# Kernel optimization log

Hardware: AMD Instinct MI355X
Metric: run time of the kernel (lower is better)

Reference implementation:

```python
import jax, jax.numpy as jnp
import numpy as np

B, N, K = 4, 4096, 10   # batch, num points, ED_nsample
SA, ED = 128, 4          # SA_conv_out, ED_conv_out


def _bn_pack(key, C):
    # rows: gamma, beta, running_mean, running_var (eval-mode BatchNorm1d)
    kg, kb, km, kv = jax.random.split(key, 4)
    g = 1.0 + 0.1 * jax.random.normal(kg, (C,))
    b = 0.1 * jax.random.normal(kb, (C,))
    m = 0.1 * jax.random.normal(km, (C,))
    v = jax.random.uniform(kv, (C,), minval=0.5, maxval=1.5)
    return jnp.stack([g, b, m, v])


def _conv_params(key, o, c):
    kw, kb = jax.random.split(key)
    return (jax.random.normal(kw, (o, c)) * (1.0 / np.sqrt(c)),
            0.01 * jax.random.normal(kb, (o,)))


def setup_inputs() -> dict:
    key = jax.random.key(0)
    ks = iter(jax.random.split(key, 32))
    inp = {}
    inp['pointcloud'] = jax.random.normal(next(ks), (B, N, 3), dtype=jnp.float32)
    inp['h1'] = jax.random.normal(next(ks), (B, SA, N), dtype=jnp.float32)      # Pointnet_Backbone output
    inp['h2'] = jax.random.normal(next(ks), (B, 1024, N), dtype=jnp.float32)    # DGCNN output
    shapes = {'dg1': (256, 1024), 'dg2': (64, 256), 'dg3': (32, 64),
              'c1': (512, 160), 'c2': (256, 512), 'c3': (128, 256), 'f': (128, 132)}
    for name, (o, c) in shapes.items():
        W, b = _conv_params(next(ks), o, c)
        inp['W_' + name], inp['b_' + name] = W, b
        inp['bn_' + name] = _bn_pack(next(ks), o)
    inp['W_ed1'] = jax.random.normal(next(ks), (ED, 3)) * 0.5
    inp['b_ed1'] = 0.01 * jax.random.normal(next(ks), (ED,))
    inp['W_ed2'] = jax.random.normal(next(ks), (ED, ED)) * 0.5
    inp['b_ed2'] = 0.01 * jax.random.normal(next(ks), (ED,))
    inp['numpoints'] = N
    return inp


def _bn1d(x, p, eps=1e-5):
    # x: [B, C, N]; p rows: gamma, beta, mean, var
    g, b, m, v = p
    inv = g * jax.lax.rsqrt(v + eps)
    return x * inv[:, None] + (b - m * inv)[:, None]


def _conv1(x, W, b):
    # 1x1 Conv1d == channel matmul. x: [B,C,N], W: [O,C]
    return jnp.einsum('oc,bcn->bon', W, x) + b[:, None]


def reference(pointcloud, h1, h2,
              W_dg1, b_dg1, bn_dg1, W_dg2, b_dg2, bn_dg2, W_dg3, b_dg3, bn_dg3,
              W_c1, b_c1, bn_c1, W_c2, b_c2, bn_c2, W_c3, b_c3, bn_c3,
              W_f, b_f, bn_f, W_ed1, b_ed1, W_ed2, b_ed2, numpoints):
    relu = jax.nn.relu
    xyz = pointcloud[..., :3]  # [B,N,3]

    # DGCNN feature reduction: 1024 -> 256 -> 64 -> 32
    h2_ = relu(_bn1d(_conv1(h2, W_dg1, b_dg1), bn_dg1))
    h2_ = relu(_bn1d(_conv1(h2_, W_dg2, b_dg2), bn_dg2))
    h2_ = relu(_bn1d(_conv1(h2_, W_dg3, b_dg3), bn_dg3))

    # fused feature: 160 -> 512 -> 256 -> 128
    f = jnp.concatenate([h1, h2_], axis=1)
    f_ = relu(_bn1d(_conv1(f, W_c1, b_c1), bn_c1))
    f_ = relu(_bn1d(_conv1(f_, W_c2, b_c2), bn_c2))
    f_ = relu(_bn1d(_conv1(f_, W_c3, b_c3), bn_c3))

    # knn_point: K nearest neighbors of each point within its cloud
    sq = jnp.sum(xyz * xyz, axis=-1)  # [B,N]
    d = sq[:, :, None] + sq[:, None, :] - 2.0 * jnp.einsum('bnd,bmd->bnm', xyz, xyz)
    _, idx = jax.lax.top_k(-d, K)  # [B,N,K]
    nbr = jax.vmap(lambda p, i: p[i])(xyz, idx)  # [B,N,K,3]

    # per-point 3x3 covariance + eigenvalues
    c = nbr - jnp.mean(nbr, axis=2, keepdims=True)
    cov = jnp.einsum('bnki,bnkj->bnij', c, c) / K  # [B,N,3,3]
    ev = jnp.linalg.eigvalsh(cov)  # [B,N,3] ascending

    # sub3_ED: Linear(3,4) -> ReLU -> Linear(4,4)
    ef = relu(ev @ W_ed1.T + b_ed1) @ W_ed2.T + b_ed2  # [B,N,4]
    ef_t = ef.transpose(0, 2, 1)  # [B,4,N]

    z = jnp.concatenate([f_, ef_t], axis=1)  # [B,132,N]
    z_ = relu(_bn1d(_conv1(z, W_f, b_f), bn_f))  # [B,128,N]
    return (xyz, z_, h1, h2_, ef_t)
```

## Files before the change

kernel.cpp:

```cpp
#include <hip/hip_runtime.h>
#include <hip/hip_bf16.h>
#include <math.h>

typedef __hip_bfloat16 bf16;

#define BB 4
#define NN 4096
#define KNB 10
#define KQ 8
#define KS 32
#define KC (NN / KS)
#define KCAP 64

typedef __bf16 bfv8 __attribute__((ext_vector_type(8)));
typedef float  f32x4 __attribute__((ext_vector_type(4)));

__device__ __forceinline__ float ldT(const float* p) { return *p; }
__device__ __forceinline__ float ldT(const bf16* p)  { return __bfloat162float(*p); }
__device__ __forceinline__ void  stT(float* p, float v) { *p = v; }
__device__ __forceinline__ void  stT(bf16* p,  float v) { *p = __float2bfloat16(v); }

__device__ __forceinline__ unsigned short f2us(float x) {
  union { bf16 h; unsigned short u; } cv;
  cv.h = __float2bfloat16(x);
  return cv.u;
}

__device__ __forceinline__ void ld8bits(const float* p, unsigned short* s) {
  const float4 a = *(const float4*)p;
  const float4 b = *(const float4*)(p + 4);
  s[0] = f2us(a.x); s[1] = f2us(a.y); s[2] = f2us(a.z); s[3] = f2us(a.w);
  s[4] = f2us(b.x); s[5] = f2us(b.y); s[6] = f2us(b.z); s[7] = f2us(b.w);
}
__device__ __forceinline__ void ld8bits(const bf16* p, unsigned short* s) {
  const uint2 a = *(const uint2*)p;
  const uint2 b = *(const uint2*)(p + 4);
  s[0] = a.x & 0xffff; s[1] = a.x >> 16; s[2] = a.y & 0xffff; s[3] = a.y >> 16;
  s[4] = b.x & 0xffff; s[5] = b.x >> 16; s[6] = b.y & 0xffff; s[7] = b.y >> 16;
}

__device__ __forceinline__ bfv8 ldfrag(const unsigned short* p) {
  union { uint4 u; bfv8 v; } t;
  t.u = *(const uint4*)p;
  return t.v;
}

__global__ void k_sniff(const unsigned int* __restrict__ pcw, int* __restrict__ flag) {
  if (blockIdx.x == 0 && threadIdx.x == 0) {
    int hits = 0;
    for (int i = 0; i < 64; ++i) {
      unsigned int e = (pcw[i] >> 7) & 0xFF;
      if (e >= 100 && e <= 140) ++hits;
    }
    *flag = (hits >= 40) ? 1 : 0;
  }
}

template <class TI, class TO>
__global__ void k_prep(const int* __restrict__ flag, int want,
                       const TI* __restrict__ pc, float* __restrict__ xyz,
                       float4* __restrict__ pts4, TO* __restrict__ out0) {
  if (flag && *flag != want) return;
  int i = blockIdx.x * blockDim.x + threadIdx.x;
  if (i >= BB * NN) return;
  float x = ldT(pc + i * 3 + 0), y = ldT(pc + i * 3 + 1), z = ldT(pc + i * 3 + 2);
  xyz[i * 3 + 0] = x; xyz[i * 3 + 1] = y; xyz[i * 3 + 2] = z;
  const float nrm = fmaf(x, x, fmaf(y, y, z * z));
  pts4[i] = make_float4(x, y, z, nrm);
  stT(out0 + i * 3 + 0, x); stT(out0 + i * 3 + 1, y); stT(out0 + i * 3 + 2, z);
}

template <class TI, class TO>
__global__ void k_h1(const int* __restrict__ flag, int want,
                     const TI* __restrict__ h1, TO* __restrict__ out2,
                     bf16* __restrict__ fbuf) {
  if (flag && *flag != want) return;
  int i = blockIdx.x * blockDim.x + threadIdx.x;
  const int per = 128 * NN;
  if (i >= BB * per) return;
  float v = ldT(h1 + i);
  stT(out2 + i, v);
  int b = i / per, r = i - b * per;
  fbuf[(size_t)b * 160 * NN + r] = __float2bfloat16(v);
}

__global__ __launch_bounds__(256, 8) void k_knn(const float4* __restrict__ pts4,
                                                int* __restrict__ idxout) {
  __shared__ float sminb[KS][KQ];
  __shared__ float stau[KQ];
  __shared__ float sd[KQ][KCAP];
  __shared__ int   si[KQ][KCAP];
  __shared__ unsigned int scnt[KQ];
  const int tid = threadIdx.x;
  const int q = tid & (KQ - 1);
  const int s = tid >> 3;
  const int n = blockIdx.x * KQ + q;
  const int b = blockIdx.y;
  const float4* pb = pts4 + (size_t)b * NN;
  const float4 pq = pb[n];
  const float xn = pq.x, yn = pq.y, zn = pq.z, sn = pq.w;
  if (tid < KQ) scnt[tid] = 0u;

  const float4* cp = pb + s * KC;
  float mv[8];
  #pragma unroll
  for (int u = 0; u < 8; ++u) mv[u] = 1e30f;
  for (int j = 0; j < KC; j += 8) {
    #pragma unroll
    for (int u = 0; u < 8; ++u) {
      const float4 c = cp[j + u];
      const float dot = fmaf(xn, c.x, fmaf(yn, c.y, zn * c.z));
      const float d = (sn + c.w) - 2.0f * dot;
      mv[u] = fminf(mv[u], d);
    }
  }
  {
    const float a0 = fminf(fminf(mv[0], mv[1]), fminf(mv[2], mv[3]));
    const float a1 = fminf(fminf(mv[4], mv[5]), fminf(mv[6], mv[7]));
    sminb[s][q] = fminf(a0, a1);
  }
  __syncthreads();

  if (tid < KQ) {
    float arr[KNB];
    #pragma unroll
    for (int t = 0; t < KNB; ++t) arr[t] = 1e30f;
    #pragma unroll
    for (int ss = 0; ss < KS; ++ss) {
      const float v = sminb[ss][tid];
      if (v < arr[KNB - 1]) {
        arr[KNB - 1] = v;
        #pragma unroll
        for (int t = KNB - 1; t > 0; --t)
          if (arr[t] < arr[t - 1]) { const float tm = arr[t]; arr[t] = arr[t - 1]; arr[t - 1] = tm; }
      }
    }
    stau[tid] = arr[KNB - 1];
  }
  __syncthreads();
  const float tau = stau[q];

  for (int j = 0; j < KC; j += 4) {
    #pragma unroll
    for (int u = 0; u < 4; ++u) {
      const float4 c = cp[j + u];
      const float dot = fmaf(xn, c.x, fmaf(yn, c.y, zn * c.z));
      const float d = (sn + c.w) - 2.0f * dot;
      if (d <= tau) {
        const unsigned int pos = atomicAdd(&scnt[q], 1u);
        if (pos < KCAP) { sd[q][pos] = d; si[q][pos] = s * KC + j + u; }
      }
    }
  }
  __syncthreads();

  if (tid < KQ) {
    const int qq = tid;
    const int nq = blockIdx.x * KQ + qq;
    int* op = idxout + ((size_t)b * NN + nq) * KNB;
    const unsigned int m = scnt[qq];
    float dk[KNB]; int ik[KNB];
    #pragma unroll
    for (int t = 0; t < KNB; ++t) { dk[t] = 1e30f; ik[t] = NN; }
    if (m <= KCAP) {
      for (unsigned int e = 0; e < m; ++e) {
        const float d = sd[qq][e];
        const int j = si[qq][e];
        if (d < dk[KNB - 1] || (d == dk[KNB - 1] && j < ik[KNB - 1])) {
          dk[KNB - 1] = d; ik[KNB - 1] = j;
          #pragma unroll
          for (int t = KNB - 1; t > 0; --t) {
            if (dk[t] < dk[t - 1] || (dk[t] == dk[t - 1] && ik[t] < ik[t - 1])) {
              const float td = dk[t]; dk[t] = dk[t - 1]; dk[t - 1] = td;
              const int ti = ik[t]; ik[t] = ik[t - 1]; ik[t - 1] = ti;
            }
          }
        }
      }
    } else {
      const float4 pQ = pb[nq];
      for (int j = 0; j < NN; ++j) {
        const float4 c = pb[j];
        const float dot = fmaf(pQ.x, c.x, fmaf(pQ.y, c.y, pQ.z * c.z));
        const float d = (pQ.w + c.w) - 2.0f * dot;
        if (d < dk[KNB - 1] || (d == dk[KNB - 1] && j < ik[KNB - 1])) {
          dk[KNB - 1] = d; ik[KNB - 1] = j;
          #pragma unroll
          for (int t = KNB - 1; t > 0; --t) {
            if (dk[t] < dk[t - 1] || (dk[t] == dk[t - 1] && ik[t] < ik[t - 1])) {
              const float td = dk[t]; dk[t] = dk[t - 1]; dk[t - 1] = td;
              const int ti = ik[t]; ik[t] = ik[t - 1]; ik[t - 1] = ti;
            }
          }
        }
      }
    }
    #pragma unroll
    for (int t = 0; t < KNB; ++t) op[t] = ik[t];
  }
}

template <class TP, class TO>
__global__ void k_ef(const int* __restrict__ flag, int want,
                     const float* __restrict__ xyz, const int* __restrict__ idxin,
                     const TP* __restrict__ W1, const TP* __restrict__ b1,
                     const TP* __restrict__ W2, const TP* __restrict__ b2,
                     TO* __restrict__ out4, bf16* __restrict__ zbuf) {
  if (flag && *flag != want) return;
  int i = blockIdx.x * blockDim.x + threadIdx.x;
  if (i >= BB * NN) return;
  int b = i / NN, n = i - b * NN;
  const float* xb = xyz + (size_t)b * NN * 3;
  const int* id = idxin + (size_t)i * KNB;
  double px[KNB], py[KNB], pz[KNB];
  double mx = 0, my = 0, mz = 0;
  #pragma unroll
  for (int k = 0; k < KNB; ++k) {
    int j = id[k];
    px[k] = (double)xb[j * 3 + 0];
    py[k] = (double)xb[j * 3 + 1];
    pz[k] = (double)xb[j * 3 + 2];
    mx += px[k]; my += py[k]; mz += pz[k];
  }
  mx /= KNB; my /= KNB; mz /= KNB;
  double c00 = 0, c01 = 0, c02 = 0, c11 = 0, c12 = 0, c22 = 0;
  #pragma unroll
  for (int k = 0; k < KNB; ++k) {
    double dx = px[k] - mx, dy = py[k] - my, dz = pz[k] - mz;
    c00 += dx * dx; c01 += dx * dy; c02 += dx * dz;
    c11 += dy * dy; c12 += dy * dz; c22 += dz * dz;
  }
  c00 /= KNB; c01 /= KNB; c02 /= KNB; c11 /= KNB; c12 /= KNB; c22 /= KNB;
  double e0, e1, e2;
  {
    double p1 = c01 * c01 + c02 * c02 + c12 * c12;
    double q = (c00 + c11 + c22) / 3.0;
    double d0 = c00 - q, d1 = c11 - q, d2 = c22 - q;
    double p2 = d0 * d0 + d1 * d1 + d2 * d2 + 2.0 * p1;
    if (p2 <= 0.0) {
      e0 = e1 = e2 = q;
    } else {
      double p = sqrt(p2 / 6.0);
      double ip = 1.0 / p;
      double b00 = d0 * ip, b11 = d1 * ip, b22 = d2 * ip;
      double b01 = c01 * ip, b02 = c02 * ip, b12 = c12 * ip;
      double det = b00 * (b11 * b22 - b12 * b12)
                 - b01 * (b01 * b22 - b12 * b02)
                 + b02 * (b01 * b12 - b11 * b02);
      double r = 0.5 * det;
      r = fmin(1.0, fmax(-1.0, r));
      double phi = acos(r) / 3.0;
      double lmax = q + 2.0 * p * cos(phi);
      double lmin = q + 2.0 * p * cos(phi + 2.0943951023931953);
      e0 = lmin; e2 = lmax; e1 = 3.0 * q - lmax - lmin;
    }
  }
  float ev0 = (float)e0, ev1 = (float)e1, ev2 = (float)e2;
  float h[4];
  #pragma unroll
  for (int o = 0; o < 4; ++o) {
    float t = ev0 * ldT(W1 + o * 3 + 0) + ev1 * ldT(W1 + o * 3 + 1)
            + ev2 * ldT(W1 + o * 3 + 2) + ldT(b1 + o);
    h[o] = fmaxf(t, 0.f);
  }
  #pragma unroll
  for (int j = 0; j < 4; ++j) {
    float t = h[0] * ldT(W2 + j * 4 + 0) + h[1] * ldT(W2 + j * 4 + 1)
            + h[2] * ldT(W2 + j * 4 + 2) + h[3] * ldT(W2 + j * 4 + 3)
            + ldT(b2 + j);
    stT(out4 + ((size_t)b * 4 + j) * NN + n, t);
    zbuf[((size_t)b * 132 + 128 + j) * NN + n] = __float2bfloat16(t);
  }
}

template <class TX, class TP, class TO>
__global__ __launch_bounds__(256) void k_gemm(
    const int* __restrict__ flag, int want,
    const TX* __restrict__ X, int C,
    const TP* __restrict__ W, const TP* __restrict__ bias,
    const TP* __restrict__ bn, int O,
    TO* __restrict__ Yout, int YRo, int yoffo,
    bf16* __restrict__ Ybuf, int YRb, int yoffb) {
  if (flag && *flag != want) return;
  __shared__ __align__(16) unsigned short Ws[64][72];
  __shared__ __align__(16) unsigned short Xs[64][72];
  const int tid  = threadIdx.x;
  const int lane = tid & 63;
  const int wv   = tid >> 6;
  const int wr = wv >> 1, wc = wv & 1;
  const int l15 = lane & 15, lg = lane >> 4;
  const int nBase = blockIdx.x * 64;
  const int oBase = blockIdx.y * 64;
  const int b = blockIdx.z;
  const TX* Xb = X + (size_t)b * C * NN;

  f32x4 acc[2][2];
  #pragma unroll
  for (int m = 0; m < 2; ++m)
    #pragma unroll
    for (int n = 0; n < 2; ++n) acc[m][n] = (f32x4){0.f, 0.f, 0.f, 0.f};

  const int wo  = tid >> 3;
  const int wc0 = (tid & 7) << 3;
  const int xc  = tid >> 3;
  const int xn0 = (tid & 7) << 3;

  for (int cb = 0; cb < C; cb += 64) {
    #pragma unroll
    for (int h = 0; h < 2; ++h) {
      const int o  = wo + h * 32;
      const int go = oBase + o, gc = cb + wc0;
      const int crem = C - gc;
      unsigned short s[8];
      if (go < O && crem >= 8) {
        ld8bits(W + (size_t)go * C + gc, s);
      } else {
        #pragma unroll
        for (int j = 0; j < 8; ++j)
          s[j] = (go < O && j < crem) ? f2us(ldT(W + (size_t)go * C + gc + j))
                                      : (unsigned short)0;
      }
      uint4 u;
      u.x = (unsigned)s[0] | ((unsigned)s[1] << 16);
      u.y = (unsigned)s[2] | ((unsigned)s[3] << 16);
      u.z = (unsigned)s[4] | ((unsigned)s[5] << 16);
      u.w = (unsigned)s[6] | ((unsigned)s[7] << 16);
      *(uint4*)&Ws[o][wc0] = u;
    }
    #pragma unroll
    for (int h = 0; h < 2; ++h) {
      const int c  = xc + h * 32;
      const int gc = cb + c;
      unsigned short s[8];
      if (gc < C) {
        ld8bits(Xb + (size_t)gc * NN + nBase + xn0, s);
      } else {
        #pragma unroll
        for (int j = 0; j < 8; ++j) s[j] = 0;
      }
      const int xcol = c ^ xn0;
      #pragma unroll
      for (int j = 0; j < 8; ++j) Xs[xn0 + j][xcol] = s[j];
    }
    __syncthreads();
    #pragma unroll
    for (int kk = 0; kk < 2; ++kk) {
      bfv8 af[2], xf[2];
      #pragma unroll
      for (int m = 0; m < 2; ++m)
        af[m] = ldfrag(&Ws[wr * 32 + m * 16 + l15][kk * 32 + lg * 8]);
      #pragma unroll
      for (int n = 0; n < 2; ++n) {
        const int nl  = wc * 32 + n * 16 + l15;
        const int col = (kk * 32 + lg * 8) ^ (((nl >> 3) & 7) << 3);
        xf[n] = ldfrag(&Xs[nl][col]);
      }
      #pragma unroll
      for (int m = 0; m < 2; ++m)
        #pragma unroll
        for (int n = 0; n < 2; ++n)
          acc[m][n] = __builtin_amdgcn_mfma_f32_16x16x32_bf16(af[m], xf[n], acc[m][n], 0, 0, 0);
    }
    __syncthreads();
  }

  #pragma unroll
  for (int m = 0; m < 2; ++m) {
    const int ob = oBase + wr * 32 + m * 16 + lg * 4;
    #pragma unroll
    for (int r = 0; r < 4; ++r) {
      const int oo = ob + r;
      if (oo >= O) continue;
      const float bc  = ldT(bias + oo);
      const float g   = ldT(bn + oo);
      const float bbv = ldT(bn + O + oo);
      const float mm  = ldT(bn + 2 * O + oo);
      const float vv  = ldT(bn + 3 * O + oo);
      const float inv = g / sqrtf(vv + 1e-5f);
      const float sh  = bbv - mm * inv;
      #pragma unroll
      for (int n = 0; n < 2; ++n) {
        const int nn2 = nBase + wc * 32 + n * 16 + l15;
        const float rv = fmaxf((acc[m][n][r] + bc) * inv + sh, 0.f);
        if (Yout) stT(Yout + ((size_t)b * YRo + yoffo + oo) * NN + nn2, rv);
        if (Ybuf) Ybuf[((size_t)b * YRb + yoffb + oo) * NN + nn2] = __float2bfloat16(rv);
      }
    }
  }
}

template <class TI>
static void launch_prep(int want, const int* flag, void* const* d_in, void* d_out,
                        hipStream_t stream, float* xyz, float4* pts4) {
  typedef TI TO;
  const TI* pc = (const TI*)d_in[0];
  TO* out0 = (TO*)d_out;
  k_prep<TI, TO><<<dim3((BB * NN + 255) / 256), 256, 0, stream>>>(flag, want, pc, xyz, pts4, out0);
}

template <class TI>
static void launch_rest(int want, const int* flag,
                        void* const* d_in, void* d_out, hipStream_t stream,
                        float* xyz, int* idx,
                        bf16* t512, bf16* t256, bf16* t64, bf16* fbuf, bf16* zbuf) {
  typedef TI TO;
  const TI* h1    = (const TI*)d_in[1];
  const TI* h2    = (const TI*)d_in[2];
  const TI* W_dg1 = (const TI*)d_in[3];  const TI* b_dg1 = (const TI*)d_in[4];  const TI* bn_dg1 = (const TI*)d_in[5];
  const TI* W_dg2 = (const TI*)d_in[6];  const TI* b_dg2 = (const TI*)d_in[7];  const TI* bn_dg2 = (const TI*)d_in[8];
  const TI* W_dg3 = (const TI*)d_in[9];  const TI* b_dg3 = (const TI*)d_in[10]; const TI* bn_dg3 = (const TI*)d_in[11];
  const TI* W_c1  = (const TI*)d_in[12]; const TI* b_c1  = (const TI*)d_in[13]; const TI* bn_c1  = (const TI*)d_in[14];
  const TI* W_c2  = (const TI*)d_in[15]; const TI* b_c2  = (const TI*)d_in[16]; const TI* bn_c2  = (const TI*)d_in[17];
  const TI* W_c3  = (const TI*)d_in[18]; const TI* b_c3  = (const TI*)d_in[19]; const TI* bn_c3  = (const TI*)d_in[20];
  const TI* W_f   = (const TI*)d_in[21]; const TI* b_f   = (const TI*)d_in[22]; const TI* bn_f   = (const TI*)d_in[23];
  const TI* W_ed1 = (const TI*)d_in[24]; const TI* b_ed1 = (const TI*)d_in[25];
  const TI* W_ed2 = (const TI*)d_in[26]; const TI* b_ed2 = (const TI*)d_in[27];

  TO* out  = (TO*)d_out;
  TO* out1 = out + 49152;
  TO* out2 = out1 + 2097152;
  TO* out3 = out2 + 2097152;
  TO* out4 = out3 + 524288;

  dim3 blk(256);
  k_h1<TI, TO><<<dim3((BB * 128 * NN + 255) / 256), 256, 0, stream>>>(flag, want, h1, out2, fbuf);
  k_gemm<TI, TI, TO><<<dim3(64, 4, BB), blk, 0, stream>>>(flag, want, h2, 1024, W_dg1, b_dg1, bn_dg1, 256,
                                                          (TO*)nullptr, 0, 0, t256, 256, 0);
  k_gemm<bf16, TI, TO><<<dim3(64, 1, BB), blk, 0, stream>>>(flag, want, t256, 256, W_dg2, b_dg2, bn_dg2, 64,
                                                            (TO*)nullptr, 0, 0, t64, 64, 0);
  k_gemm<bf16, TI, TO><<<dim3(64, 1, BB), blk, 0, stream>>>(flag, want, t64, 64, W_dg3, b_dg3, bn_dg3, 32,
                                                            out3, 32, 0, fbuf, 160, 128);
  k_gemm<bf16, TI, TO><<<dim3(64, 8, BB), blk, 0, stream>>>(flag, want, fbuf, 160, W_c1, b_c1, bn_c1, 512,
                                                            (TO*)nullptr, 0, 0, t512, 512, 0);
  k_ef<TI, TO><<<dim3((BB * NN + 255) / 256), 256, 0, stream>>>(flag, want, xyz, idx, W_ed1, b_ed1, W_ed2, b_ed2, out4, zbuf);
  k_gemm<bf16, TI, TO><<<dim3(64, 4, BB), blk, 0, stream>>>(flag, want, t512, 512, W_c2, b_c2, bn_c2, 256,
                                                            (TO*)nullptr, 0, 0, t256, 256, 0);
  k_gemm<bf16, TI, TO><<<dim3(64, 2, BB), blk, 0, stream>>>(flag, want, t256, 256, W_c3, b_c3, bn_c3, 128,
                                                            (TO*)nullptr, 0, 0, zbuf, 132, 0);
  k_gemm<bf16, TI, TO><<<dim3(64, 2, BB), blk, 0, stream>>>(flag, want, zbuf, 132, W_f, b_f, bn_f, 128,
                                                            out1, 128, 0, (bf16*)nullptr, 0, 0);
}

extern "C" void kernel_launch(void* const* d_in, const int* in_sizes, int n_in,
                              void* d_out, int out_size, void* d_ws, size_t ws_size,
                              hipStream_t stream) {
  char* ws = (char*)d_ws;
  int*    flag = (int*)(ws + 0);
  float*  xyz  = (float*)(ws + 1024);
  int*    idx  = (int*)(ws + 328704);
  bf16*   t512 = (bf16*)(ws + 1048576);
  bf16*   t256 = (bf16*)(ws + 17825792);
  bf16*   t64  = (bf16*)(ws + 26214400);
  bf16*   fbuf = (bf16*)(ws + 28311552);
  bf16*   zbuf = (bf16*)(ws + 33554432);
  float4* pts4 = (float4*)(ws + 1048576);

  int mode = -1;
  if (in_sizes) {
    if (in_sizes[0] == (int)(BB * NN * 3 * sizeof(float))) mode = 0;
    else if (in_sizes[0] == (int)(BB * NN * 3 * sizeof(bf16))) mode = 1;
  }

  if (mode < 0) {
    k_sniff<<<1, 64, 0, stream>>>((const unsigned int*)d_in[0], flag);
    launch_prep<float>(0, flag, d_in, d_out, stream, xyz, pts4);
    launch_prep<bf16>(1, flag, d_in, d_out, stream, xyz, pts4);
  } else if (mode == 0) {
    launch_prep<float>(0, nullptr, d_in, d_out, stream, xyz, pts4);
  } else {
    launch_prep<bf16>(1, nullptr, d_in, d_out, stream, xyz, pts4);
  }

  k_knn<<<dim3(NN / KQ, BB), 256, 0, stream>>>(pts4, idx);

  if (mode != 1) launch_rest<float>(0, mode < 0 ? flag : nullptr, d_in, d_out, stream,
                                    xyz, idx, t512, t256, t64, fbuf, zbuf);
  if (mode != 0) launch_rest<bf16>(1, mode < 0 ? flag : nullptr, d_in, d_out, stream,
                                   xyz, idx, t512, t256, t64, fbuf, zbuf);
}
```

Measured before the change: 394.1 us.

## Restructure kNN so each thread scans strided candidates against all block queries

The kNN kernel now has each thread load a strided candidate point once and compute distances against all 8 queries of the block held in registers. Before, each thread handled one query over a contiguous chunk. Candidate loads become coalesced and each load is reused across queries, cutting global or cache traffic. In exchange, the threshold pass now reduces 256 per-thread minima per query instead of 32, serialized in 8 threads. Register pressure also rises, so launch bounds drop from 8 to 6 blocks per CU.

```diff
diff --git a/kernel.cpp b/kernel.cpp
--- a/kernel.cpp
+++ b/kernel.cpp
@@ -8,8 +8,6 @@
 #define NN 4096
 #define KNB 10
 #define KQ 8
-#define KS 32
-#define KC (NN / KS)
 #define KCAP 64
 
 typedef __bf16 bfv8 __attribute__((ext_vector_type(8)));
@@ -84,71 +82,76 @@
   fbuf[(size_t)b * 160 * NN + r] = __float2bfloat16(v);
 }
 
-__global__ __launch_bounds__(256, 8) void k_knn(const float4* __restrict__ pts4,
+__global__ __launch_bounds__(256, 6) void k_knn(const float4* __restrict__ pts4,
                                                 int* __restrict__ idxout) {
-  __shared__ float sminb[KS][KQ];
+  __shared__ float smin[256][KQ + 1];
   __shared__ float stau[KQ];
   __shared__ float sd[KQ][KCAP];
   __shared__ int   si[KQ][KCAP];
   __shared__ unsigned int scnt[KQ];
+  __shared__ float4 sq[KQ];
   const int tid = threadIdx.x;
-  const int q = tid & (KQ - 1);
-  const int s = tid >> 3;
-  const int n = blockIdx.x * KQ + q;
   const int b = blockIdx.y;
+  const int nBase = blockIdx.x * KQ;
   const float4* pb = pts4 + (size_t)b * NN;
-  const float4 pq = pb[n];
-  const float xn = pq.x, yn = pq.y, zn = pq.z, sn = pq.w;
-  if (tid < KQ) scnt[tid] = 0u;
-
-  const float4* cp = pb + s * KC;
-  float mv[8];
-  #pragma unroll
-  for (int u = 0; u < 8; ++u) mv[u] = 1e30f;
-  for (int j = 0; j < KC; j += 8) {
-    #pragma unroll
-    for (int u = 0; u < 8; ++u) {
-      const float4 c = cp[j + u];
-      const float dot = fmaf(xn, c.x, fmaf(yn, c.y, zn * c.z));
-      const float d = (sn + c.w) - 2.0f * dot;
-      mv[u] = fminf(mv[u], d);
-    }
-  }
-  {
-    const float a0 = fminf(fminf(mv[0], mv[1]), fminf(mv[2], mv[3]));
-    const float a1 = fminf(fminf(mv[4], mv[5]), fminf(mv[6], mv[7]));
-    sminb[s][q] = fminf(a0, a1);
-  }
+  if (tid < KQ) { sq[tid] = pb[nBase + tid]; scnt[tid] = 0u; }
+  __syncthreads();
+
+  float qx[KQ], qy[KQ], qz[KQ], qn[KQ];
+  #pragma unroll
+  for (int q = 0; q < KQ; ++q) {
+    const float4 p = sq[q];
+    qx[q] = p.x; qy[q] = p.y; qz[q] = p.z; qn[q] = p.w;
+  }
+
+  float mv[KQ];
+  #pragma unroll
+  for (int q = 0; q < KQ; ++q) mv[q] = 1e30f;
+  #pragma unroll 4
+  for (int it = 0; it < 16; ++it) {
+    const float4 c = pb[it * 256 + tid];
+    #pragma unroll
+    for (int q = 0; q < KQ; ++q) {
+      const float dot = fmaf(qx[q], c.x, fmaf(qy[q], c.y, qz[q] * c.z));
+      const float d = (qn[q] + c.w) - 2.0f * dot;
+      mv[q] = fminf(mv[q], d);
+    }
+  }
+  #pragma unroll
+  for (int q = 0; q < KQ; ++q) smin[tid][q] = mv[q];
   __syncthreads();
 
   if (tid < KQ) {
     float arr[KNB];
     #pragma unroll
     for (int t = 0; t < KNB; ++t) arr[t] = 1e30f;
-    #pragma unroll
-    for (int ss = 0; ss < KS; ++ss) {
-      const float v = sminb[ss][tid];
+    for (int t = 0; t < 256; ++t) {
+      const float v = smin[t][tid];
       if (v < arr[KNB - 1]) {
         arr[KNB - 1] = v;
         #pragma unroll
-        for (int t = KNB - 1; t > 0; --t)
-          if (arr[t] < arr[t - 1]) { const float tm = arr[t]; arr[t] = arr[t - 1]; arr[t - 1] = tm; }
+        for (int u = KNB - 1; u > 0; --u)
+          if (arr[u] < arr[u - 1]) { const float tm = arr[u]; arr[u] = arr[u - 1]; arr[u - 1] = tm; }
       }
     }
     stau[tid] = arr[KNB - 1];
   }
   __syncthreads();
-  const float tau = stau[q];
-
-  for (int j = 0; j < KC; j += 4) {
-    #pragma unroll
-    for (int u = 0; u < 4; ++u) {
-      const float4 c = cp[j + u];
-      const float dot = fmaf(xn, c.x, fmaf(yn, c.y, zn * c.z));
-      const float d = (sn + c.w) - 2.0f * dot;
-      if (d <= tau) {
+  float tq[KQ];
+  #pragma unroll
+  for (int q = 0; q < KQ; ++q) tq[q] = stau[q];
+
+  #pragma unroll 4
+  for (int it = 0; it < 16; ++it) {
+    const float4 c = pb[it * 256 + tid];
+    const int j = it * 256 + tid;
+    #pragma unroll
+    for (int q = 0; q < KQ; ++q) {
+      const float dot = fmaf(qx[q], c.x, fmaf(qy[q], c.y, qz[q] * c.z));
+      const float d = (qn[q] + c.w) - 2.0f * dot;
+      if (d <= tq[q]) {
         const unsigned int pos = atomicAdd(&scnt[q], 1u);
-        if (pos < KCAP) { sd[q][pos] = d; si[q][pos] = s * KC + j + u; }
+        if (pos < KCAP) { sd[q][pos] = d; si[q][pos] = j; }
       }
     }
   }
@@ -156,7 +159,7 @@
 
   if (tid < KQ) {
     const int qq = tid;
-    const int nq = blockIdx.x * KQ + qq;
+    const int nq = nBase + qq;
     int* op = idxout + ((size_t)b * NN + nq) * KNB;
     const unsigned int m = scnt[qq];
     float dk[KNB]; int ik[KNB];
```

New measurement: 409.6 us. 3.9% more time.
